# Optimization experiments

Measured on AMD Instinct MI355X. Metric: run time of the kernel, lower is better.

The kernel has to match this reference:

```python
import jax, jax.numpy as jnp
import numpy as np

N = 10000
E = 640000
C = 128   # in_channels
H = 512   # hidden_dim
O = 128   # out_channels


def setup_inputs() -> dict:
    key = jax.random.key(0)
    k1, k2, k3, k4, k5, k6, k7 = jax.random.split(key, 7)
    x = jax.random.normal(k1, (N, C), dtype=jnp.float32)
    edge_index = jax.random.randint(k2, (2, E), 0, N, dtype=jnp.int64)
    # MLP params (Linear(2C, H) -> ReLU -> Linear(H, O)), torch default init scale
    w1 = jax.random.uniform(k3, (2 * C, H), jnp.float32, -1, 1) / np.sqrt(2 * C)
    b1 = jax.random.uniform(k4, (H,), jnp.float32, -1, 1) / np.sqrt(2 * C)
    w2 = jax.random.uniform(k5, (H, O), jnp.float32, -1, 1) / np.sqrt(H)
    b2 = jax.random.uniform(k6, (O,), jnp.float32, -1, 1) / np.sqrt(H)
    return {"x": x, "edge_index": edge_index, "w1": w1, "b1": b1, "w2": w2, "b2": b2}


def reference(x, edge_index, w1, b1, w2, b2):
    row, col = edge_index[0], edge_index[1]
    # scatter_mean: mean of source features x[col] into destination row
    summed = jax.ops.segment_sum(x[col], row, num_segments=N)          # [N, C]
    count = jax.ops.segment_sum(jnp.ones((E,), x.dtype), row, num_segments=N)
    neighbor_mean = summed / jnp.maximum(count, 1.0)[:, None]          # [N, C]
    h = jnp.concatenate([x, neighbor_mean], axis=1)                    # [N, 2C]
    h = jax.nn.relu(h @ w1 + b1)                                       # [N, H]
    return h @ w2 + b2                                                 # [N, O]
```

## Files before the change

kernel.cpp:

```cpp
#include <hip/hip_runtime.h>

#define C_IN 128
#define H_DIM 512
#define O_DIM 128
#define CAP   192
#define PAD   16

typedef __attribute__((ext_vector_type(8))) short short8;
typedef __attribute__((ext_vector_type(4))) float f32x4;

__device__ inline unsigned short f2bf(float f) {
    unsigned int u = __float_as_uint(f);
    unsigned int r = (u + 0x7FFF + ((u >> 16) & 1)) >> 16;
    return (unsigned short)r;
}

__global__ void zero_kernel(int4* __restrict__ cnt_p4, int n4) {
    int idx = blockIdx.x * blockDim.x + threadIdx.x;
    if (idx < n4) cnt_p4[idx] = make_int4(0, 0, 0, 0);
}

__global__ void fill_kernel(const int* __restrict__ ei, int* __restrict__ cnt_p,
                            int* __restrict__ bucket, int E) {
    int e = blockIdx.x * blockDim.x + threadIdx.x;
    if (e >= E) return;
    int row = ei[e];
    int col = ei[E + e];
    int slot = atomicAdd(&cnt_p[row * PAD], 1);
    if (slot < CAP) bucket[row * CAP + slot] = col;
}

__global__ __launch_bounds__(256)
void gather_kernel(const float* __restrict__ x, const int* __restrict__ bucket,
                   const int* __restrict__ cnt_p, unsigned short* __restrict__ h0,
                   int N) {
    const int lane = threadIdx.x & 63;
    const int n = blockIdx.x * 4 + (threadIdx.x >> 6);
    if (n >= N) return;
    const int half = lane >> 5;
    const int l32 = lane & 31;
    const int degt = cnt_p[n * PAD];
    const int deg = min(degt, CAP);
    const int base = n * CAP;

    float4 acc = make_float4(0.f, 0.f, 0.f, 0.f);
    int e = 0;
    for (; e + 4 <= deg; e += 4) {
        int c0 = bucket[base + e + half];
        int c1 = bucket[base + e + 2 + half];
        float4 v0 = *(const float4*)(x + (long)c0 * C_IN + l32 * 4);
        float4 v1 = *(const float4*)(x + (long)c1 * C_IN + l32 * 4);
        acc.x += v0.x + v1.x;
        acc.y += v0.y + v1.y;
        acc.z += v0.z + v1.z;
        acc.w += v0.w + v1.w;
    }
    for (; e + 2 <= deg; e += 2) {
        int c = bucket[base + e + half];
        float4 v = *(const float4*)(x + (long)c * C_IN + l32 * 4);
        acc.x += v.x; acc.y += v.y; acc.z += v.z; acc.w += v.w;
    }
    if (e < deg && half == 0) {
        int c = bucket[base + e];
        float4 v = *(const float4*)(x + (long)c * C_IN + l32 * 4);
        acc.x += v.x; acc.y += v.y; acc.z += v.z; acc.w += v.w;
    }
    acc.x += __shfl_xor(acc.x, 32, 64);
    acc.y += __shfl_xor(acc.y, 32, 64);
    acc.z += __shfl_xor(acc.z, 32, 64);
    acc.w += __shfl_xor(acc.w, 32, 64);

    unsigned short* dst = h0 + (long)n * (2 * C_IN);
    if (half == 0) {
        float inv = 1.0f / fmaxf((float)degt, 1.0f);
        ushort4 mv;
        mv.x = f2bf(acc.x * inv);
        mv.y = f2bf(acc.y * inv);
        mv.z = f2bf(acc.z * inv);
        mv.w = f2bf(acc.w * inv);
        *(ushort4*)(dst + C_IN + l32 * 4) = mv;
    } else {
        float4 self = *(const float4*)(x + (long)n * C_IN + l32 * 4);
        ushort4 sv;
        sv.x = f2bf(self.x);
        sv.y = f2bf(self.y);
        sv.z = f2bf(self.z);
        sv.w = f2bf(self.w);
        *(ushort4*)(dst + l32 * 4) = sv;
    }
}

__device__ inline void tr_tile(const float* __restrict__ src, unsigned short* __restrict__ dst,
                               int R, int Ccols, int bx, int by) {
    __shared__ float tile[32][33];
    const int c0 = bx * 32, r0 = by * 32;
    const int tx = threadIdx.x & 31, ty = threadIdx.x >> 5;
#pragma unroll
    for (int i = 0; i < 32; i += 8)
        tile[ty + i][tx] = src[(long)(r0 + ty + i) * Ccols + c0 + tx];
    __syncthreads();
#pragma unroll
    for (int i = 0; i < 32; i += 8)
        dst[(long)(c0 + ty + i) * R + r0 + tx] = f2bf(tile[tx][ty + i]);
}

__global__ __launch_bounds__(256)
void transpose_cvt2(const float* __restrict__ w1, unsigned short* __restrict__ w1t,
                    const float* __restrict__ w2, unsigned short* __restrict__ w2t) {
    if (blockIdx.z == 0) {
        if (blockIdx.x < H_DIM / 32 && blockIdx.y < (2 * C_IN) / 32)
            tr_tile(w1, w1t, 2 * C_IN, H_DIM, blockIdx.x, blockIdx.y);
    } else {
        if (blockIdx.x < O_DIM / 32 && blockIdx.y < H_DIM / 32)
            tr_tile(w2, w2t, H_DIM, O_DIM, blockIdx.x, blockIdx.y);
    }
}

template <bool RELU, bool OUT_BF16>
__global__ __launch_bounds__(256)
void gemm_mfma(const unsigned short* __restrict__ A, const unsigned short* __restrict__ Bt,
               const float* __restrict__ bias, void* __restrict__ Cmat,
               int M, int K, int Nw) {
    __shared__ __align__(16) unsigned short As[64][72];
    __shared__ __align__(16) unsigned short Bs[64][72];

    const int t = threadIdx.x;
    const int m0 = blockIdx.y * 64;
    const int n0 = blockIdx.x * 64;

    const int lane = t & 63;
    const int w = t >> 6;
    const int wm = (w >> 1) * 32;
    const int wn = (w & 1) * 32;
    const int l16 = lane & 15;
    const int q8 = (lane >> 4) * 8;

    const int sr = t >> 3;
    const int sc = (t & 7) * 8;

    f32x4 acc[2][2] = {};

    for (int k0 = 0; k0 < K; k0 += 64) {
        {
            int gm = m0 + sr;
            short8 v = {};
            if (gm < M) v = *(const short8*)(A + (long)gm * K + k0 + sc);
            *(short8*)&As[sr][sc] = v;
            gm = m0 + sr + 32;
            short8 v2 = {};
            if (gm < M) v2 = *(const short8*)(A + (long)gm * K + k0 + sc);
            *(short8*)&As[sr + 32][sc] = v2;
        }
        {
            int gn = n0 + sr;
            *(short8*)&Bs[sr][sc] = *(const short8*)(Bt + (long)gn * K + k0 + sc);
            gn = n0 + sr + 32;
            *(short8*)&Bs[sr + 32][sc] = *(const short8*)(Bt + (long)gn * K + k0 + sc);
        }
        __syncthreads();

#pragma unroll
        for (int kk = 0; kk < 64; kk += 32) {
            short8 a0 = *(const short8*)&As[wm + l16][kk + q8];
            short8 a1 = *(const short8*)&As[wm + 16 + l16][kk + q8];
            short8 b0 = *(const short8*)&Bs[wn + l16][kk + q8];
            short8 b1 = *(const short8*)&Bs[wn + 16 + l16][kk + q8];
            acc[0][0] = __builtin_amdgcn_mfma_f32_16x16x32_bf16(a0, b0, acc[0][0], 0, 0, 0);
            acc[0][1] = __builtin_amdgcn_mfma_f32_16x16x32_bf16(a0, b1, acc[0][1], 0, 0, 0);
            acc[1][0] = __builtin_amdgcn_mfma_f32_16x16x32_bf16(a1, b0, acc[1][0], 0, 0, 0);
            acc[1][1] = __builtin_amdgcn_mfma_f32_16x16x32_bf16(a1, b1, acc[1][1], 0, 0, 0);
        }
        __syncthreads();
    }

    const int rbase = (lane >> 4) * 4;
#pragma unroll
    for (int mi = 0; mi < 2; mi++) {
#pragma unroll
        for (int ni = 0; ni < 2; ni++) {
            int gn = n0 + wn + ni * 16 + l16;
            float bb = bias[gn];
#pragma unroll
            for (int r = 0; r < 4; r++) {
                int gm = m0 + wm + mi * 16 + rbase + r;
                if (gm >= M) continue;
                float v = acc[mi][ni][r] + bb;
                if (RELU) v = fmaxf(v, 0.f);
                if (OUT_BF16)
                    ((unsigned short*)Cmat)[(long)gm * Nw + gn] = f2bf(v);
                else
                    ((float*)Cmat)[(long)gm * Nw + gn] = v;
            }
        }
    }
}

extern "C" void kernel_launch(void* const* d_in, const int* in_sizes, int n_in,
                              void* d_out, int out_size, void* d_ws, size_t ws_size,
                              hipStream_t stream) {
    const float* x  = (const float*)d_in[0];
    const int*   ei = (const int*)d_in[1];
    const float* w1 = (const float*)d_in[2];
    const float* b1 = (const float*)d_in[3];
    const float* w2 = (const float*)d_in[4];
    const float* b2 = (const float*)d_in[5];
    float* out = (float*)d_out;

    const int N = in_sizes[0] / C_IN;
    const int E = in_sizes[1] / 2;

    unsigned short* h0b = (unsigned short*)d_ws;
    unsigned short* h1b = h0b + (size_t)N * (2 * C_IN);
    unsigned short* w1t = h1b + (size_t)N * H_DIM;
    unsigned short* w2t = w1t + (size_t)H_DIM * (2 * C_IN);
    int* cnt_p = (int*)(w2t + (size_t)O_DIM * H_DIM);
    int* bucket = cnt_p + (size_t)N * PAD;

    int n4 = N * PAD / 4;
    zero_kernel<<<(n4 + 255) / 256, 256, 0, stream>>>((int4*)cnt_p, n4);
    fill_kernel<<<(E + 255) / 256, 256, 0, stream>>>(ei, cnt_p, bucket, E);
    gather_kernel<<<(N + 3) / 4, 256, 0, stream>>>(x, bucket, cnt_p, h0b, N);
    transpose_cvt2<<<dim3(16, 16, 2), 256, 0, stream>>>(w1, w1t, w2, w2t);

    dim3 g1(H_DIM / 64, (N + 63) / 64);
    gemm_mfma<true, true><<<g1, 256, 0, stream>>>(h0b, w1t, b1, h1b, N, 2 * C_IN, H_DIM);

    dim3 g2(O_DIM / 64, (N + 63) / 64);
    gemm_mfma<false, false><<<g2, 256, 0, stream>>>(h1b, w2t, b2, out, N, H_DIM, O_DIM);
}
```

Baseline: 156.9 us.

## Gather neighbors from bf16 copy of x, use 16-bit bucket indices, fuse prep kernels

A single prep kernel now writes bf16 x into the first half of h0, zeroes the counters and transposes both weight matrices, replacing three launches with one. The gather then reads neighbor features as bf16 from h0 instead of fp32 x, which halves the bytes per random row read. Bucket indices are stored as unsigned short, halving bucket traffic. This assumes N fits in 16 bits and sums bf16-rounded inputs, so the neighbor mean carries slightly more rounding error.

```diff
diff --git a/kernel.cpp b/kernel.cpp
--- a/kernel.cpp
+++ b/kernel.cpp
@@ -14,24 +14,62 @@
     unsigned int r = (u + 0x7FFF + ((u >> 16) & 1)) >> 16;
     return (unsigned short)r;
 }
-
-__global__ void zero_kernel(int4* __restrict__ cnt_p4, int n4) {
-    int idx = blockIdx.x * blockDim.x + threadIdx.x;
-    if (idx < n4) cnt_p4[idx] = make_int4(0, 0, 0, 0);
+__device__ inline float bf2f(unsigned short s) {
+    return __uint_as_float(((unsigned int)s) << 16);
+}
+
+__device__ inline void tr_tile(const float* __restrict__ src, unsigned short* __restrict__ dst,
+                               int R, int Ccols, int bx, int by) {
+    __shared__ float tile[32][33];
+    const int c0 = bx * 32, r0 = by * 32;
+    const int tx = threadIdx.x & 31, ty = threadIdx.x >> 5;
+#pragma unroll
+    for (int i = 0; i < 32; i += 8)
+        tile[ty + i][tx] = src[(long)(r0 + ty + i) * Ccols + c0 + tx];
+    __syncthreads();
+#pragma unroll
+    for (int i = 0; i < 32; i += 8)
+        dst[(long)(c0 + ty + i) * R + r0 + tx] = f2bf(tile[tx][ty + i]);
+}
+
+__global__ __launch_bounds__(256)
+void prep_kernel(const float* __restrict__ w1, unsigned short* __restrict__ w1t,
+                 const float* __restrict__ w2, unsigned short* __restrict__ w2t,
+                 const float* __restrict__ x, unsigned short* __restrict__ h0,
+                 int* __restrict__ cnt_p, int N) {
+    if (blockIdx.z == 0) {
+        if (blockIdx.y < (2 * C_IN) / 32) tr_tile(w1, w1t, 2 * C_IN, H_DIM, blockIdx.x, blockIdx.y);
+    } else if (blockIdx.z == 1) {
+        if (blockIdx.x < O_DIM / 32) tr_tile(w2, w2t, H_DIM, O_DIM, blockIdx.x, blockIdx.y);
+    } else {
+        const int bid = blockIdx.y * 16 + blockIdx.x;
+        const int gtid = bid * 256 + threadIdx.x;
+        const int nf4 = N * C_IN / 4;
+        for (int i = gtid; i < nf4; i += 65536) {
+            int n = i >> 5, c4 = i & 31;
+            float4 v = ((const float4*)x)[i];
+            ushort4 s;
+            s.x = f2bf(v.x); s.y = f2bf(v.y); s.z = f2bf(v.z); s.w = f2bf(v.w);
+            *(ushort4*)(h0 + (long)n * (2 * C_IN) + c4 * 4) = s;
+        }
+        const int n4 = N * PAD / 4;
+        for (int i = gtid; i < n4; i += 65536)
+            ((int4*)cnt_p)[i] = make_int4(0, 0, 0, 0);
+    }
 }
 
 __global__ void fill_kernel(const int* __restrict__ ei, int* __restrict__ cnt_p,
-                            int* __restrict__ bucket, int E) {
+                            unsigned short* __restrict__ bucket, int E) {
     int e = blockIdx.x * blockDim.x + threadIdx.x;
     if (e >= E) return;
     int row = ei[e];
     int col = ei[E + e];
     int slot = atomicAdd(&cnt_p[row * PAD], 1);
-    if (slot < CAP) bucket[row * CAP + slot] = col;
+    if (slot < CAP) bucket[(long)row * CAP + slot] = (unsigned short)col;
 }
 
 __global__ __launch_bounds__(256)
-void gather_kernel(const float* __restrict__ x, const int* __restrict__ bucket,
+void gather_kernel(const unsigned short* __restrict__ bucket,
                    const int* __restrict__ cnt_p, unsigned short* __restrict__ h0,
                    int N) {
     const int lane = threadIdx.x & 63;
@@ -41,78 +79,43 @@
     const int l32 = lane & 31;
     const int degt = cnt_p[n * PAD];
     const int deg = min(degt, CAP);
-    const int base = n * CAP;
-
-    float4 acc = make_float4(0.f, 0.f, 0.f, 0.f);
+    const long base = (long)n * CAP;
+
+    float a0 = 0.f, a1 = 0.f, a2 = 0.f, a3 = 0.f;
     int e = 0;
     for (; e + 4 <= deg; e += 4) {
         int c0 = bucket[base + e + half];
         int c1 = bucket[base + e + 2 + half];
-        float4 v0 = *(const float4*)(x + (long)c0 * C_IN + l32 * 4);
-        float4 v1 = *(const float4*)(x + (long)c1 * C_IN + l32 * 4);
-        acc.x += v0.x + v1.x;
-        acc.y += v0.y + v1.y;
-        acc.z += v0.z + v1.z;
-        acc.w += v0.w + v1.w;
+        ushort4 u0 = *(const ushort4*)(h0 + (long)c0 * (2 * C_IN) + l32 * 4);
+        ushort4 u1 = *(const ushort4*)(h0 + (long)c1 * (2 * C_IN) + l32 * 4);
+        a0 += bf2f(u0.x) + bf2f(u1.x);
+        a1 += bf2f(u0.y) + bf2f(u1.y);
+        a2 += bf2f(u0.z) + bf2f(u1.z);
+        a3 += bf2f(u0.w) + bf2f(u1.w);
     }
     for (; e + 2 <= deg; e += 2) {
         int c = bucket[base + e + half];
-        float4 v = *(const float4*)(x + (long)c * C_IN + l32 * 4);
-        acc.x += v.x; acc.y += v.y; acc.z += v.z; acc.w += v.w;
+        ushort4 u = *(const ushort4*)(h0 + (long)c * (2 * C_IN) + l32 * 4);
+        a0 += bf2f(u.x); a1 += bf2f(u.y); a2 += bf2f(u.z); a3 += bf2f(u.w);
     }
     if (e < deg && half == 0) {
         int c = bucket[base + e];
-        float4 v = *(const float4*)(x + (long)c * C_IN + l32 * 4);
-        acc.x += v.x; acc.y += v.y; acc.z += v.z; acc.w += v.w;
-    }
-    acc.x += __shfl_xor(acc.x, 32, 64);
-    acc.y += __shfl_xor(acc.y, 32, 64);
-    acc.z += __shfl_xor(acc.z, 32, 64);
-    acc.w += __shfl_xor(acc.w, 32, 64);
-
-    unsigned short* dst = h0 + (long)n * (2 * C_IN);
+        ushort4 u = *(const ushort4*)(h0 + (long)c * (2 * C_IN) + l32 * 4);
+        a0 += bf2f(u.x); a1 += bf2f(u.y); a2 += bf2f(u.z); a3 += bf2f(u.w);
+    }
+    a0 += __shfl_xor(a0, 32, 64);
+    a1 += __shfl_xor(a1, 32, 64);
+    a2 += __shfl_xor(a2, 32, 64);
+    a3 += __shfl_xor(a3, 32, 64);
+
     if (half == 0) {
         float inv = 1.0f / fmaxf((float)degt, 1.0f);
         ushort4 mv;
-        mv.x = f2bf(acc.x * inv);
-        mv.y = f2bf(acc.y * inv);
-        mv.z = f2bf(acc.z * inv);
-        mv.w = f2bf(acc.w * inv);
-        *(ushort4*)(dst + C_IN + l32 * 4) = mv;
-    } else {
-        float4 self = *(const float4*)(x + (long)n * C_IN + l32 * 4);
-        ushort4 sv;
-        sv.x = f2bf(self.x);
-        sv.y = f2bf(self.y);
-        sv.z = f2bf(self.z);
-        sv.w = f2bf(self.w);
-        *(ushort4*)(dst + l32 * 4) = sv;
-    }
-}
-
-__device__ inline void tr_tile(const float* __restrict__ src, unsigned short* __restrict__ dst,
-                               int R, int Ccols, int bx, int by) {
-    __shared__ float tile[32][33];
-    const int c0 = bx * 32, r0 = by * 32;
-    const int tx = threadIdx.x & 31, ty = threadIdx.x >> 5;
-#pragma unroll
-    for (int i = 0; i < 32; i += 8)
-        tile[ty + i][tx] = src[(long)(r0 + ty + i) * Ccols + c0 + tx];
-    __syncthreads();
-#pragma unroll
-    for (int i = 0; i < 32; i += 8)
-        dst[(long)(c0 + ty + i) * R + r0 + tx] = f2bf(tile[tx][ty + i]);
-}
-
-__global__ __launch_bounds__(256)
-void transpose_cvt2(const float* __restrict__ w1, unsigned short* __restrict__ w1t,
-                    const float* __restrict__ w2, unsigned short* __restrict__ w2t) {
-    if (blockIdx.z == 0) {
-        if (blockIdx.x < H_DIM / 32 && blockIdx.y < (2 * C_IN) / 32)
-            tr_tile(w1, w1t, 2 * C_IN, H_DIM, blockIdx.x, blockIdx.y);
-    } else {
-        if (blockIdx.x < O_DIM / 32 && blockIdx.y < H_DIM / 32)
-            tr_tile(w2, w2t, H_DIM, O_DIM, blockIdx.x, blockIdx.y);
+        mv.x = f2bf(a0 * inv);
+        mv.y = f2bf(a1 * inv);
+        mv.z = f2bf(a2 * inv);
+        mv.w = f2bf(a3 * inv);
+        *(ushort4*)(h0 + (long)n * (2 * C_IN) + C_IN + l32 * 4) = mv;
     }
 }
 
@@ -214,13 +217,11 @@
     unsigned short* w1t = h1b + (size_t)N * H_DIM;
     unsigned short* w2t = w1t + (size_t)H_DIM * (2 * C_IN);
     int* cnt_p = (int*)(w2t + (size_t)O_DIM * H_DIM);
-    int* bucket = cnt_p + (size_t)N * PAD;
-
-    int n4 = N * PAD / 4;
-    zero_kernel<<<(n4 + 255) / 256, 256, 0, stream>>>((int4*)cnt_p, n4);
+    unsigned short* bucket = (unsigned short*)(cnt_p + (size_t)N * PAD);
+
+    prep_kernel<<<dim3(16, 16, 3), 256, 0, stream>>>(w1, w1t, w2, w2t, x, h0b, cnt_p, N);
     fill_kernel<<<(E + 255) / 256, 256, 0, stream>>>(ei, cnt_p, bucket, E);
-    gather_kernel<<<(N + 3) / 4, 256, 0, stream>>>(x, bucket, cnt_p, h0b, N);
-    transpose_cvt2<<<dim3(16, 16, 2), 256, 0, stream>>>(w1, w1t, w2, w2t);
+    gather_kernel<<<(N + 3) / 4, 256, 0, stream>>>(bucket, cnt_p, h0b, N);
 
     dim3 g1(H_DIM / 64, (N + 63) / 64);
     gemm_mfma<true, true><<<g1, 256, 0, stream>>>(h0b, w1t, b1, h1b, N, 2 * C_IN, H_DIM);
```

Result: faster. 145.6 us (-7.2%).
